# Performance work log

Measured on AMD Instinct MI355X. Metric: run time of the kernel, lower is better.

## Reference

```python
import jax, jax.numpy as jnp
import numpy as np

NH, DK, DV, KC = 12, 64, 128, 4  # heads, head_qk_dim, head_v_dim, conv_size


def causal_dwconv(x, w):
    # x: [B, L, C], w: [C, K] depthwise causal conv (torch Conv1d groups=C with left pad K-1)
    K = w.shape[1]
    L = x.shape[1]
    xp = jnp.pad(x, ((0, 0), (K - 1, 0), (0, 0)))
    out = xp[:, 0:L, :] * w[:, 0]
    for j in range(1, K):
        out = out + xp[:, j:j + L, :] * w[:, j]
    return out


def l2norm(x, eps=1e-12):
    n = jnp.sqrt(jnp.sum(x * x, axis=-1, keepdims=True))
    return x / jnp.maximum(n, eps)


def rmsnorm(x, eps=1e-5):
    return x * jax.lax.rsqrt(jnp.mean(x * x, axis=-1, keepdims=True) + eps)


def setup_inputs() -> dict:
    key = jax.random.key(0)
    ks = jax.random.split(key, 16)
    B, L, H = 4, 2048, 1024
    Kd, Vd = 768, 1536  # key_dim, value_dim
    s = 0.02
    inp = {
        'hidden_states': jax.random.normal(ks[0], (B, L, H), jnp.float32),
        'Wq': jax.random.normal(ks[1], (H, Kd), jnp.float32) * s,
        'Wk': jax.random.normal(ks[2], (H, Kd), jnp.float32) * s,
        'Wv': jax.random.normal(ks[3], (H, Vd), jnp.float32) * s,
        'Wg': jax.random.normal(ks[4], (H, Vd), jnp.float32) * s,
        'Wgk': jax.random.normal(ks[5], (H, NH), jnp.float32) * s,
        'Wb': jax.random.normal(ks[6], (H, NH), jnp.float32) * s,
        'bb': jnp.zeros((NH,), jnp.float32),
        'conv_q': jax.random.normal(ks[7], (Kd, KC), jnp.float32) * 0.3,
        'conv_k': jax.random.normal(ks[8], (Kd, KC), jnp.float32) * 0.3,
        'conv_v': jax.random.normal(ks[9], (Vd, KC), jnp.float32) * 0.3,
        'A_log': jnp.log(jax.random.uniform(ks[10], (NH,), jnp.float32, 1e-4, 16.0)),
        'gnorm_w': jnp.ones((DV,), jnp.float32),
        'Wo': jax.random.normal(ks[11], (Vd, H), jnp.float32) * s,
    }
    dt = jnp.exp(jax.random.uniform(ks[12], (NH,), jnp.float32) * (np.log(0.1) - np.log(0.001)) + np.log(0.001))
    dt = jnp.clip(dt, 1e-4, None)
    inp['dt_bias'] = dt + jnp.log(-jnp.expm1(-dt))
    return inp


def reference(hidden_states, Wq, Wk, Wv, Wg, Wgk, Wb, bb, conv_q, conv_k, conv_v, A_log, dt_bias, gnorm_w, Wo):
    B, L, H = hidden_states.shape
    # projections + causal depthwise short conv with silu (qk_norm='l2')
    q = jax.nn.silu(causal_dwconv(hidden_states @ Wq, conv_q))
    k = jax.nn.silu(causal_dwconv(hidden_states @ Wk, conv_k))
    v = jax.nn.silu(causal_dwconv(hidden_states @ Wv, conv_v))
    # mamba-style decay gate: gk = -exp(A_log) * softplus(x Wgk + dt_bias)  -> [B,L,NH]
    gk = -jnp.exp(A_log) * jax.nn.softplus(hidden_states @ Wgk + dt_bias)
    beta = jax.nn.sigmoid(hidden_states @ Wb + bb)  # [B,L,NH]
    q = l2norm(q.reshape(B, L, NH, DK))
    k = l2norm(k.reshape(B, L, NH, DK))
    v = v.reshape(B, L, NH, DV)

    # gated delta rule recurrence: S_t = exp(gk_t) * S_{t-1}; S_t += k_t (beta_t (v_t - k_t^T S_t)); o_t = q_t^T S_t
    def step(S, inp_t):
        qt, kt, vt, gt, bt = inp_t
        S = S * jnp.exp(gt)[..., None, None]
        pred = jnp.einsum('bhk,bhkv->bhv', kt, S)
        delta = bt[..., None] * (vt - pred)
        S = S + kt[..., None] * delta[:, :, None, :]
        ot = jnp.einsum('bhk,bhkv->bhv', qt, S)
        return S, ot

    xs = (jnp.moveaxis(q, 1, 0), jnp.moveaxis(k, 1, 0), jnp.moveaxis(v, 1, 0),
          jnp.moveaxis(gk, 1, 0), jnp.moveaxis(beta, 1, 0))
    S0 = jnp.zeros((B, NH, DK, DV), hidden_states.dtype)
    _, o = jax.lax.scan(step, S0, xs)
    o = jnp.moveaxis(o, 0, 1)  # [B,L,NH,DV]

    # fused RMSNorm + swish gate, then output projection
    g = (hidden_states @ Wg).reshape(B, L, NH, DV)
    o = rmsnorm(o) * gnorm_w * jax.nn.silu(g)
    return o.reshape(B, L, NH * DV) @ Wo
```

## Files before the change

kernel.cpp:

```cpp
#include <hip/hip_runtime.h>

#define B_   4
#define L_   2048
#define H_   1024
#define KD   768
#define VD   1536
#define NHh  12
#define DKh  64
#define DVh  128
#define M_   (B_ * L_)
#define NC   32
#define NCID (B_ * NHh * NC)

using bf16x8 = __attribute__((ext_vector_type(8))) __bf16;
using f32x4  = __attribute__((ext_vector_type(4))) float;
using ui4    = __attribute__((ext_vector_type(4))) unsigned int;
using f4v    = __attribute__((ext_vector_type(4))) float;
using u16x4  = __attribute__((ext_vector_type(4))) unsigned short;
using u16x8  = __attribute__((ext_vector_type(8))) unsigned short;

__device__ __forceinline__ float bf2f(unsigned short u) {
  unsigned int x = ((unsigned int)u) << 16;
  return __builtin_bit_cast(float, x);
}
__device__ __forceinline__ unsigned short f2bf(float f) {
  unsigned int u = __builtin_bit_cast(unsigned int, f);
  u += 0x7fffu + ((u >> 16) & 1u);
  return (unsigned short)(u >> 16);
}
__device__ __forceinline__ float sigmoidf_(float x) { return 1.f / (1.f + __expf(-x)); }

__device__ __forceinline__ void async_copy16(const unsigned short* __restrict__ g,
                                             unsigned short* l) {
  __builtin_amdgcn_global_load_lds((const __attribute__((address_space(1))) unsigned int*)g,
                                   (__attribute__((address_space(3))) unsigned int*)l, 16, 0, 0);
}

__global__ void detect_dtype(const unsigned short* __restrict__ hs, int* __restrict__ flag) {
  int tid = threadIdx.x;
  int cnt = 0;
  for (int i = tid; i < 1024; i += 256) {
    int e = (hs[i] >> 7) & 0xFF;
    if (e >= 134) cnt++;
  }
  #pragma unroll
  for (int off = 32; off; off >>= 1) cnt += __shfl_xor(cnt, off);
  __shared__ int red[4];
  if ((tid & 63) == 0) red[tid >> 6] = cnt;
  __syncthreads();
  if (tid == 0) *flag = (red[0] + red[1] + red[2] + red[3] > 100) ? 1 : 0;
}

__global__ void convert_hs4(const void* __restrict__ src, unsigned short* __restrict__ dst,
                            const int* __restrict__ flag) {
  size_t i = ((size_t)blockIdx.x * 256 + threadIdx.x) * 4;
  if (*flag) {
    f4v v = *(const f4v*)((const float*)src + i);
    u16x4 o;
    o.x = f2bf(v[0]); o.y = f2bf(v[1]); o.z = f2bf(v[2]); o.w = f2bf(v[3]);
    *(u16x4*)(dst + i) = o;
  } else {
    *(u16x4*)(dst + i) = *(const u16x4*)((const unsigned short*)src + i);
  }
}

__global__ void convert_small(const void* s0, const void* s1, const void* s2,
                              const void* s3, const void* s4, const void* s5, const void* s6,
                              float* d0, float* d1, float* d2, float* d3, float* d4,
                              float* d5, float* d6, const int* __restrict__ flag) {
  const int sizes[7] = {KD * 4, KD * 4, VD * 4, NHh, NHh, NHh, DVh};
  int a = blockIdx.y;
  const void* s; float* d;
  switch (a) {
    case 0: s = s0; d = d0; break;  case 1: s = s1; d = d1; break;
    case 2: s = s2; d = d2; break;  case 3: s = s3; d = d3; break;
    case 4: s = s4; d = d4; break;  case 5: s = s5; d = d5; break;
    default: s = s6; d = d6; break;
  }
  int i = blockIdx.x * 256 + threadIdx.x;
  if (i >= sizes[a]) return;
  float v = (*flag) ? ((const float*)s)[i] : bf2f(((const unsigned short*)s)[i]);
  if (a < 3) {
    int C = (a == 2) ? VD : KD;
    d[(i & 3) * C + (i >> 2)] = v;
  } else {
    d[i] = v;
  }
}

__global__ void transpose_conv(const void* __restrict__ in, unsigned short* __restrict__ out,
                               int R, int C, const int* __restrict__ flag) {
  __shared__ unsigned short tile[32][33];
  int f = *flag;
  int c0 = blockIdx.x * 32, r0 = blockIdx.y * 32;
  int tx = threadIdx.x & 31, ty = threadIdx.x >> 5;
  #pragma unroll
  for (int i = 0; i < 32; i += 8) {
    int r = r0 + ty + i, c = c0 + tx;
    unsigned short v = 0;
    if (r < R && c < C)
      v = f ? f2bf(((const float*)in)[(size_t)r * C + c])
            : ((const unsigned short*)in)[(size_t)r * C + c];
    tile[ty + i][tx] = v;
  }
  __syncthreads();
  #pragma unroll
  for (int i = 0; i < 32; i += 8) {
    int c = c0 + ty + i, r = r0 + tx;
    if (c < C && r < R) out[(size_t)c * R + r] = tile[tx][ty + i];
  }
}

#define BMt 128
#define BNt 128
#define BKt 64

__global__ __launch_bounds__(256, 2) void gemm_bt(
    const unsigned short* __restrict__ Ag,
    const unsigned short* __restrict__ BTg,
    void* __restrict__ Cg,
    int M, int N, int K, int f32mode, const int* __restrict__ flag) {
  __shared__ __align__(16) unsigned short As[2][BMt * BKt];
  __shared__ __align__(16) unsigned short Bs[2][BNt * BKt];
  const int tid = threadIdx.x;
  const int wave = tid >> 6, lane = tid & 63;
  const int wr = wave >> 1, wc = wave & 1;
  const int lrow = lane & 15, lq = lane >> 4;
  const int row0 = blockIdx.x * BMt;
  const int bcol0 = blockIdx.y * BNt;
  unsigned short* Cb = (unsigned short*)Cg;
  int col0 = bcol0, Nst = N;
  if (f32mode == 3) {
    int region = bcol0 / 1536;
    Cb += (size_t)region * (size_t)M_ * 1536;
    col0 = bcol0 - region * 1536;
    Nst = 1536;
  }
  f32x4 acc[4][4] = {};
  auto stage = [&](int sb, int k0) {
    #pragma unroll
    for (int i = 0; i < 4; i++) {
      int c = i * 256 + tid;
      int r = c >> 3;
      int kk = ((c & 7) ^ (r & 7)) << 3;
      int ldsbase = (i * 256 + wave * 64) * 8;
      async_copy16(&Ag[(size_t)(row0 + r) * K + k0 + kk], &As[sb][ldsbase]);
      async_copy16(&BTg[(size_t)(bcol0 + r) * K + k0 + kk], &Bs[sb][ldsbase]);
    }
  };
  stage(0, 0);
  __syncthreads();
  int cur = 0;
  for (int k0 = 0; k0 < K; k0 += BKt) {
    if (k0 + BKt < K) stage(cur ^ 1, k0 + BKt);
    #pragma unroll
    for (int ks = 0; ks < BKt; ks += 32) {
      bf16x8 af[4], bfr[4];
      #pragma unroll
      for (int i = 0; i < 4; i++) {
        int ra = wr * 64 + i * 16 + lrow;
        int sa = ((ks >> 3) + lq) ^ (ra & 7);
        af[i]  = *(const bf16x8*)&As[cur][ra * BKt + (sa << 3)];
        int rb = wc * 64 + i * 16 + lrow;
        int sb2 = ((ks >> 3) + lq) ^ (rb & 7);
        bfr[i] = *(const bf16x8*)&Bs[cur][rb * BKt + (sb2 << 3)];
      }
      #pragma unroll
      for (int mi = 0; mi < 4; mi++)
        #pragma unroll
        for (int ni = 0; ni < 4; ni++)
          acc[mi][ni] = __builtin_amdgcn_mfma_f32_16x16x32_bf16(af[mi], bfr[ni], acc[mi][ni], 0, 0, 0);
    }
    __syncthreads();
    cur ^= 1;
  }
  bool f32 = (f32mode == 1) || (f32mode == 2 && *flag != 0);
  #pragma unroll
  for (int mi = 0; mi < 4; mi++)
    #pragma unroll
    for (int ni = 0; ni < 4; ni++)
      #pragma unroll
      for (int r = 0; r < 4; r++) {
        int rr = row0 + wr * 64 + mi * 16 + lq * 4 + r;
        int cc = col0 + wc * 64 + ni * 16 + lrow;
        float v = acc[mi][ni][r];
        if (f32) ((float*)Cg)[(size_t)rr * N + cc] = v;
        else     Cb[(size_t)rr * Nst + cc] = f2bf(v);
      }
}

__global__ void gkbeta_kernel(const float* __restrict__ logits,
                              const float* __restrict__ bb,
                              const float* __restrict__ A_log,
                              const float* __restrict__ dt_bias,
                              float* __restrict__ gkb, float* __restrict__ betab) {
  int idx = blockIdx.x * 256 + threadIdx.x;
  int m = idx / 24, j = idx - m * 24;
  float x = logits[(size_t)m * 128 + j];
  if (j < 12) {
    float t = x + dt_bias[j];
    float sp = (t > 20.f) ? t : log1pf(__expf(t));
    gkb[m * NHh + j] = -__expf(A_log[j]) * sp;
  } else {
    betab[m * NHh + (j - 12)] = sigmoidf_(x + bb[j - 12]);
  }
}

__global__ __launch_bounds__(192) void conv_qk_kernel(
    const unsigned short* __restrict__ raw, int rstride,
    const float* __restrict__ w,
    unsigned short* __restrict__ outp) {
  int tid = threadIdx.x;
  int rib = tid / 96, within = tid - rib * 96;
  int bl = blockIdx.x * 2 + rib;
  int c = within * 8;
  int l = bl & (L_ - 1);
  float acc[8] = {};
  #pragma unroll
  for (int j = 0; j < 4; j++) {
    int ll = l - 3 + j;
    if (ll >= 0) {
      u16x8 v = *(const u16x8*)&raw[(size_t)(bl - 3 + j) * rstride + c];
      f4v w0 = *(const f4v*)&w[j * KD + c];
      f4v w1 = *(const f4v*)&w[j * KD + c + 4];
      #pragma unroll
      for (int e = 0; e < 4; e++) acc[e] += bf2f(v[e]) * w0[e];
      #pragma unroll
      for (int e = 0; e < 4; e++) acc[4 + e] += bf2f(v[4 + e]) * w1[e];
    }
  }
  float x[8], ss = 0.f;
  #pragma unroll
  for (int e = 0; e < 8; e++) {
    float a = acc[e];
    x[e] = a * sigmoidf_(a);
    ss += x[e] * x[e];
  }
  #pragma unroll
  for (int off = 1; off <= 4; off <<= 1) ss += __shfl_xor(ss, off);
  float inv = 1.f / fmaxf(sqrtf(ss), 1e-12f);
  u16x8 o;
  #pragma unroll
  for (int e = 0; e < 8; e++) o[e] = f2bf(x[e] * inv);
  *(u16x8*)&outp[(size_t)bl * KD + c] = o;
}

__global__ void conv_v_kernel(const unsigned short* __restrict__ raw,
                              const float* __restrict__ w,
                              unsigned short* __restrict__ outp) {
  int idx = blockIdx.x * 256 + threadIdx.x;
  int bl = idx / 192;
  int c = (idx - bl * 192) * 8;
  int l = bl & (L_ - 1);
  float acc[8] = {};
  #pragma unroll
  for (int j = 0; j < 4; j++) {
    int ll = l - 3 + j;
    if (ll >= 0) {
      u16x8 v = *(const u16x8*)&raw[(size_t)(bl - 3 + j) * VD + c];
      f4v w0 = *(const f4v*)&w[j * VD + c];
      f4v w1 = *(const f4v*)&w[j * VD + c + 4];
      #pragma unroll
      for (int e = 0; e < 4; e++) acc[e] += bf2f(v[e]) * w0[e];
      #pragma unroll
      for (int e = 0; e < 4; e++) acc[4 + e] += bf2f(v[4 + e]) * w1[e];
    }
  }
  u16x8 o;
  #pragma unroll
  for (int e = 0; e < 8; e++) {
    float a = acc[e];
    o[e] = f2bf(a * sigmoidf_(a));
  }
  *(u16x8*)&outp[(size_t)bl * VD + c] = o;
}

__global__ __launch_bounds__(256) void phase1_kernel(
    const unsigned short* __restrict__ kb, const unsigned short* __restrict__ vb,
    const float* __restrict__ gkb, const float* __restrict__ betab,
    unsigned short* __restrict__ U0g, unsigned short* __restrict__ Wmg,
    float* __restrict__ Gamg) {
  int cid = blockIdx.x;
  int c = cid & (NC - 1), bh = cid >> 5;
  int h = bh % NHh, b = bh / NHh;
  int bl0 = b * L_ + (c << 6);
  __shared__ __align__(16) unsigned short K_lds[64][72];
  __shared__ __align__(16) unsigned short Ab[64][72];
  __shared__ __align__(16) unsigned short Tb[64][72];
  __shared__ __align__(16) unsigned short TbT[64][72];
  __shared__ __align__(16) unsigned short Qt[64][40];
  __shared__ __align__(16) unsigned short Mpad[16][40];
  __shared__ __align__(16) unsigned short RHSt[192][72];
  __shared__ float G_lds[64], beta_lds[64], besc_lds[64];
  int tid = threadIdx.x;
  int wave = tid >> 6, lane = tid & 63, lq = lane >> 4, lrow = lane & 15;
  {
    u16x4 z = {};
    unsigned short* tb = &Tb[0][0];  unsigned short* tt = &TbT[0][0];
    for (int i = tid * 4; i < 64 * 72; i += 1024) {
      *(u16x4*)&tb[i] = z;  *(u16x4*)&tt[i] = z;
    }
    unsigned short* qt = &Qt[0][0];
    for (int i = tid * 4; i < 64 * 40; i += 1024) *(u16x4*)&qt[i] = z;
    if (tid < 160) *(u16x4*)&(&Mpad[0][0])[tid * 4] = z;
  }
  {
    int j = tid >> 2, d0 = (tid & 3) << 4;
    const ui4* src = (const ui4*)&kb[(size_t)(bl0 + j) * KD + h * 64 + d0];
    *(ui4*)&K_lds[j][d0]     = src[0];
    *(ui4*)&K_lds[j][d0 + 8] = src[1];
  }
  if (tid < 64) {
    float g  = gkb[(size_t)(bl0 + tid) * NHh + h];
    float bt = betab[(size_t)(bl0 + tid) * NHh + h];
    #pragma unroll
    for (int off = 1; off < 64; off <<= 1) {
      int src = lane - off;
      float y = __shfl(g, src < 0 ? 0 : src);
      if (lane >= off) g += y;
    }
    G_lds[tid]    = g;
    beta_lds[tid] = bt;
    besc_lds[tid] = bt * __expf(g);
    Gamg[(size_t)cid * 64 + tid] = g;
  }
  __syncthreads();
  #pragma unroll
  for (int mt = 0; mt < 4; mt++) {
    f32x4 acc = {};
    #pragma unroll
    for (int ks = 0; ks < 2; ks++) {
      bf16x8 a  = *(const bf16x8*)&K_lds[wave * 16 + lrow][ks * 32 + lq * 8];
      bf16x8 b2 = *(const bf16x8*)&K_lds[mt * 16 + lrow][ks * 32 + lq * 8];
      acc = __builtin_amdgcn_mfma_f32_16x16x32_bf16(a, b2, acc, 0, 0, 0);
    }
    #pragma unroll
    for (int r = 0; r < 4; r++) {
      int j = wave * 16 + lq * 4 + r, m = mt * 16 + lrow;
      Ab[j][m] = (m < j) ? f2bf(beta_lds[j] * __expf(G_lds[j] - G_lds[m]) * acc[r])
                         : (unsigned short)0;
    }
  }
  __syncthreads();
  if (wave == 0) {
    int blk = lq, cc = lrow, base = blk * 16;
    float t[16];
    t[0] = (cc == 0) ? 1.f : 0.f;
    #pragma unroll
    for (int j = 1; j < 16; j++) {
      float s = 0.f;
      #pragma unroll
      for (int m = 0; m < j; m++)
        s += bf2f(Ab[base + j][base + m]) * t[m];
      t[j] = ((cc == j) ? 1.f : 0.f) - s;
    }
    #pragma unroll
    for (int j = 0; j < 16; j++) {
      unsigned short bv = f2bf(t[j]);
      Tb[base + j][base + cc]  = bv;
      TbT[base + cc][base + j] = bv;
    }
  } else {
    int r = tid - 64;
    if (r < 128) {
      const unsigned short* vp = &vb[(size_t)bl0 * VD + h * 128 + r];
      for (int j = 0; j < 64; j++)
        RHSt[r][j] = f2bf(beta_lds[j] * bf2f(vp[(size_t)j * VD]));
    } else {
      int d = r - 128;
      for (int j = 0; j < 64; j++)
        RHSt[r][j] = f2bf(besc_lds[j] * bf2f(K_lds[j][d]));
    }
  }
  __syncthreads();
  #pragma unroll
  for (int lvl = 1; lvl < 4; lvl++) {
    {
      int m = tid >> 4, k = tid & 15;
      Ab[lvl * 16 + m][lvl * 16 + k] = 0;
      Mpad[m][k] = Tb[lvl * 16 + m][lvl * 16 + k];
    }
    __syncthreads();
    f32x4 accP = {};
    #pragma unroll
    for (int ks2 = 0; ks2 < 2; ks2++) {
      bf16x8 a  = *(const bf16x8*)&Ab[lvl * 16 + lrow][ks2 * 32 + lq * 8];
      bf16x8 b2 = *(const bf16x8*)&TbT[wave * 16 + lrow][ks2 * 32 + lq * 8];
      accP = __builtin_amdgcn_mfma_f32_16x16x32_bf16(a, b2, accP, 0, 0, 0);
    }
    {
      int col = wave * 16 + lrow;
      u16x4 qp;
      #pragma unroll
      for (int r = 0; r < 4; r++) {
        int krow = lq * 4 + r;
        float e = (col == lvl * 16 + krow) ? 1.f : 0.f;
        ((unsigned short*)&qp)[r] = f2bf(e - accP[r]);
      }
      *(u16x4*)&Qt[col][lq * 4] = qp;
    }
    __syncthreads();
    {
      bf16x8 am = *(const bf16x8*)&Mpad[lrow][lq * 8];
      bf16x8 bq = *(const bf16x8*)&Qt[wave * 16 + lrow][lq * 8];
      f32x4 accR = {};
      accR = __builtin_amdgcn_mfma_f32_16x16x32_bf16(am, bq, accR, 0, 0, 0);
      #pragma unroll
      for (int r = 0; r < 4; r++) {
        int row = lvl * 16 + lq * 4 + r, col = wave * 16 + lrow;
        unsigned short bv = f2bf(accR[r]);
        Tb[row][col]  = bv;
        TbT[col][row] = bv;
      }
    }
    __syncthreads();
  }
  bf16x8 af0 = *(const bf16x8*)&Tb[wave * 16 + lrow][lq * 8];
  bf16x8 af1 = *(const bf16x8*)&Tb[wave * 16 + lrow][32 + lq * 8];
  #pragma unroll
  for (int nt = 0; nt < 12; nt++) {
    f32x4 acc = {};
    bf16x8 b0 = *(const bf16x8*)&RHSt[nt * 16 + lrow][lq * 8];
    bf16x8 b1 = *(const bf16x8*)&RHSt[nt * 16 + lrow][32 + lq * 8];
    acc = __builtin_amdgcn_mfma_f32_16x16x32_bf16(af0, b0, acc, 0, 0, 0);
    acc = __builtin_amdgcn_mfma_f32_16x16x32_bf16(af1, b1, acc, 0, 0, 0);
    #pragma unroll
    for (int r = 0; r < 4; r++) {
      int i = wave * 16 + lq * 4 + r;
      int col = nt * 16 + lrow;
      if (nt < 8) U0g[(size_t)cid * 8192 + i * 128 + col] = f2bf(acc[r]);
      else        Wmg[(size_t)cid * 4096 + i * 64 + (col - 128)] = f2bf(acc[r]);
    }
  }
}

__global__ __launch_bounds__(256) void phase2_kernel(
    const unsigned short* __restrict__ kb,
    const unsigned short* __restrict__ U0g, const unsigned short* __restrict__ Wmg,
    const float* __restrict__ Gamg, unsigned short* __restrict__ P0g) {
  int blk = blockIdx.x;
  int vc = blk & 3, bh = blk >> 2;
  int h = bh % NHh, b = bh / NHh;
  __shared__ __align__(16) unsigned short P_bf[32][72];
  __shared__ __align__(16) unsigned short Wm_lds[64][72];
  __shared__ __align__(16) unsigned short Ktmp[64][72];
  __shared__ __align__(16) unsigned short KpT_lds[64][72];
  __shared__ __align__(16) unsigned short U0_lds[64][40];
  __shared__ __align__(16) unsigned short UT_lds[32][72];
  __shared__ float G2[64];
  int tid = threadIdx.x;
  int wave = tid >> 6, lane = tid & 63, lq = lane >> 4, lrow = lane & 15;
  int vt = wave & 1, dbase = (wave >> 1) * 2;
  f32x4 P[2] = {};
  int pj = tid >> 2, px = (tid & 3) << 4;
  int pv = (tid & 3) << 3;
  ui4 pf_wm0, pf_wm1, pf_k0, pf_k1, pf_u0;
  float pf_g = 0.f;
  {
    size_t cid0 = (size_t)bh * NC;
    int bl0 = b * L_;
    pf_wm0 = *(const ui4*)&Wmg[cid0 * 4096 + pj * 64 + px];
    pf_wm1 = *(const ui4*)&Wmg[cid0 * 4096 + pj * 64 + px + 8];
    pf_k0  = *(const ui4*)&kb[(size_t)(bl0 + pj) * KD + h * 64 + px];
    pf_k1  = *(const ui4*)&kb[(size_t)(bl0 + pj) * KD + h * 64 + px + 8];
    pf_u0  = *(const ui4*)&U0g[cid0 * 8192 + pj * 128 + vc * 32 + pv];
    if (tid < 64) pf_g = Gamg[cid0 * 64 + tid];
  }
  for (int c = 0; c < NC; c++) {
    size_t cid = (size_t)bh * NC + c;
    #pragma unroll
    for (int di = 0; di < 2; di++)
      #pragma unroll
      for (int r = 0; r < 4; r++)
        P_bf[vt * 16 + lq * 4 + r][(dbase + di) * 16 + lrow] = f2bf(P[di][r]);
    *(ui4*)&Wm_lds[pj][px]     = pf_wm0;
    *(ui4*)&Wm_lds[pj][px + 8] = pf_wm1;
    *(ui4*)&Ktmp[pj][px]       = pf_k0;
    *(ui4*)&Ktmp[pj][px + 8]   = pf_k1;
    *(ui4*)&U0_lds[pj][pv]     = pf_u0;
    if (tid < 64) G2[tid] = pf_g;
    __syncthreads();
    float gend = __expf(G2[63]);
    {
      int v = tid >> 3, d8 = (tid & 7) << 3;
      *(ui4*)&P0g[cid * 8192 + (size_t)(vc * 32 + v) * 64 + d8] = *(const ui4*)&P_bf[v][d8];
    }
    if (c + 1 < NC) {
      size_t cid1 = cid + 1;
      int bl1 = b * L_ + ((c + 1) << 6);
      pf_wm0 = *(const ui4*)&Wmg[cid1 * 4096 + pj * 64 + px];
      pf_wm1 = *(const ui4*)&Wmg[cid1 * 4096 + pj * 64 + px + 8];
      pf_k0  = *(const ui4*)&kb[(size_t)(bl1 + pj) * KD + h * 64 + px];
      pf_k1  = *(const ui4*)&kb[(size_t)(bl1 + pj) * KD + h * 64 + px + 8];
      pf_u0  = *(const ui4*)&U0g[cid1 * 8192 + pj * 128 + vc * 32 + pv];
      if (tid < 64) pf_g = Gamg[cid1 * 64 + tid];
    }
    {
      int d = tid & 63, j0 = (tid >> 6) << 4;
      float Ge = G2[63];
      #pragma unroll
      for (int i = 0; i < 16; i++) {
        int j = j0 + i;
        KpT_lds[d][j] = f2bf(__expf(Ge - G2[j]) * bf2f(Ktmp[j][d]));
      }
    }
    #pragma unroll
    for (int vt2 = 0; vt2 < 2; vt2++) {
      f32x4 acc = {};
      #pragma unroll
      for (int ks2 = 0; ks2 < 2; ks2++) {
        bf16x8 a  = *(const bf16x8*)&Wm_lds[wave * 16 + lrow][ks2 * 32 + lq * 8];
        bf16x8 b2 = *(const bf16x8*)&P_bf[vt2 * 16 + lrow][ks2 * 32 + lq * 8];
        acc = __builtin_amdgcn_mfma_f32_16x16x32_bf16(a, b2, acc, 0, 0, 0);
      }
      u16x4 p;
      #pragma unroll
      for (int r = 0; r < 4; r++) {
        int j = wave * 16 + lq * 4 + r;
        ((unsigned short*)&p)[r] = f2bf(bf2f(U0_lds[j][vt2 * 16 + lrow]) - acc[r]);
      }
      *(u16x4*)&UT_lds[vt2 * 16 + lrow][wave * 16 + lq * 4] = p;
    }
    __syncthreads();
    #pragma unroll
    for (int di = 0; di < 2; di++) {
      f32x4 acc = P[di];
      #pragma unroll
      for (int r = 0; r < 4; r++) acc[r] *= gend;
      #pragma unroll
      for (int ks2 = 0; ks2 < 2; ks2++) {
        bf16x8 a  = *(const bf16x8*)&UT_lds[vt * 16 + lrow][ks2 * 32 + lq * 8];
        bf16x8 b2 = *(const bf16x8*)&KpT_lds[(dbase + di) * 16 + lrow][ks2 * 32 + lq * 8];
        acc = __builtin_amdgcn_mfma_f32_16x16x32_bf16(a, b2, acc, 0, 0, 0);
      }
      P[di] = acc;
    }
  }
}

__global__ __launch_bounds__(256) void phase3_kernel(
    const unsigned short* __restrict__ qb, const unsigned short* __restrict__ kb,
    const unsigned short* __restrict__ U0g, const unsigned short* __restrict__ Wmg,
    const unsigned short* __restrict__ P0g, const float* __restrict__ Gamg,
    unsigned short* __restrict__ o_raw) {
  int cid = blockIdx.x;
  int c = cid & (NC - 1), bh = cid >> 5;
  int h = bh % NHh, b = bh / NHh;
  int bl0 = b * L_ + (c << 6);
  __shared__ __align__(16) unsigned short Q_lds[64][72];
  __shared__ __align__(16) unsigned short K_lds[64][72];
  __shared__ __align__(16) unsigned short WM_lds[64][72];
  __shared__ __align__(16) unsigned short P0_lds[128][72];
  __shared__ __align__(16) unsigned short U0_lds[64][128];
  __shared__ __align__(16) unsigned short UT_lds[128][72];
  __shared__ float G_lds[64];
  int tid = threadIdx.x;
  int wave = tid >> 6, lane = tid & 63, lq = lane >> 4, lrow = lane & 15;
  {
    int j = tid >> 2, d0 = (tid & 3) << 4;
    const ui4* qs = (const ui4*)&qb[(size_t)(bl0 + j) * KD + h * 64 + d0];
    *(ui4*)&Q_lds[j][d0] = qs[0];  *(ui4*)&Q_lds[j][d0 + 8] = qs[1];
    const ui4* ks = (const ui4*)&kb[(size_t)(bl0 + j) * KD + h * 64 + d0];
    *(ui4*)&K_lds[j][d0] = ks[0];  *(ui4*)&K_lds[j][d0 + 8] = ks[1];
    const ui4* ws = (const ui4*)&Wmg[(size_t)cid * 4096 + j * 64 + d0];
    *(ui4*)&WM_lds[j][d0] = ws[0]; *(ui4*)&WM_lds[j][d0 + 8] = ws[1];
    int v = tid >> 1, e0 = (tid & 1) << 5;
    const ui4* ps = (const ui4*)&P0g[(size_t)cid * 8192 + v * 64 + e0];
    *(ui4*)&P0_lds[v][e0]      = ps[0]; *(ui4*)&P0_lds[v][e0 + 8]  = ps[1];
    *(ui4*)&P0_lds[v][e0 + 16] = ps[2]; *(ui4*)&P0_lds[v][e0 + 24] = ps[3];
    int e1 = tid * 32;
    const ui4* us = (const ui4*)&U0g[(size_t)cid * 8192 + e1];
    ui4* ud = (ui4*)&U0_lds[0][e1];
    ud[0] = us[0]; ud[1] = us[1]; ud[2] = us[2]; ud[3] = us[3];
    if (tid < 64) G_lds[tid] = Gamg[(size_t)cid * 64 + tid];
  }
  __syncthreads();
  #pragma unroll
  for (int nt = 0; nt < 8; nt++) {
    f32x4 acc = {};
    #pragma unroll
    for (int ks2 = 0; ks2 < 2; ks2++) {
      bf16x8 a  = *(const bf16x8*)&WM_lds[wave * 16 + lrow][ks2 * 32 + lq * 8];
      bf16x8 b2 = *(const bf16x8*)&P0_lds[nt * 16 + lrow][ks2 * 32 + lq * 8];
      acc = __builtin_amdgcn_mfma_f32_16x16x32_bf16(a, b2, acc, 0, 0, 0);
    }
    u16x4 p;
    #pragma unroll
    for (int r = 0; r < 4; r++) {
      int j = wave * 16 + lq * 4 + r;
      ((unsigned short*)&p)[r] = f2bf(bf2f(U0_lds[j][nt * 16 + lrow]) - acc[r]);
    }
    *(u16x4*)&UT_lds[nt * 16 + lrow][wave * 16 + lq * 4] = p;
  }
  __syncthreads();
  #pragma unroll
  for (int mt = 0; mt < 4; mt++) {
    f32x4 acc = {};
    #pragma unroll
    for (int ks2 = 0; ks2 < 2; ks2++) {
      bf16x8 a  = *(const bf16x8*)&Q_lds[wave * 16 + lrow][ks2 * 32 + lq * 8];
      bf16x8 b2 = *(const bf16x8*)&K_lds[mt * 16 + lrow][ks2 * 32 + lq * 8];
      acc = __builtin_amdgcn_mfma_f32_16x16x32_bf16(a, b2, acc, 0, 0, 0);
    }
    #pragma unroll
    for (int r = 0; r < 4; r++) {
      int i = wave * 16 + lq * 4 + r, j = mt * 16 + lrow;
      WM_lds[i][j] = (j <= i) ? f2bf(__expf(G_lds[i] - G_lds[j]) * acc[r]) : (unsigned short)0;
    }
  }
  __syncthreads();
  #pragma unroll
  for (int nt = 0; nt < 8; nt++) {
    f32x4 accO = {}, accS = {};
    #pragma unroll
    for (int ks2 = 0; ks2 < 2; ks2++) {
      bf16x8 aM = *(const bf16x8*)&WM_lds[wave * 16 + lrow][ks2 * 32 + lq * 8];
      bf16x8 bU = *(const bf16x8*)&UT_lds[nt * 16 + lrow][ks2 * 32 + lq * 8];
      accO = __builtin_amdgcn_mfma_f32_16x16x32_bf16(aM, bU, accO, 0, 0, 0);
      bf16x8 aQ = *(const bf16x8*)&Q_lds[wave * 16 + lrow][ks2 * 32 + lq * 8];
      bf16x8 bP = *(const bf16x8*)&P0_lds[nt * 16 + lrow][ks2 * 32 + lq * 8];
      accS = __builtin_amdgcn_mfma_f32_16x16x32_bf16(aQ, bP, accS, 0, 0, 0);
    }
    #pragma unroll
    for (int r = 0; r < 4; r++) {
      int i = wave * 16 + lq * 4 + r;
      float o = accO[r] + __expf(G_lds[i]) * accS[r];
      o_raw[(size_t)(bl0 + i) * VD + h * 128 + nt * 16 + lrow] = f2bf(o);
    }
  }
}

__global__ void norm_gate_kernel(unsigned short* __restrict__ o_raw,
                                 const unsigned short* __restrict__ g,
                                 const float* __restrict__ gnw) {
  int tid = threadIdx.x;
  int r = blockIdx.x * 16 + (tid >> 4);
  int v = (tid & 15) * 8;
  u16x8 xo = *(const u16x8*)&o_raw[(size_t)r * DVh + v];
  u16x8 xg = *(const u16x8*)&g[(size_t)r * DVh + v];
  float x[8], ss = 0.f;
  #pragma unroll
  for (int e = 0; e < 8; e++) {
    x[e] = bf2f(xo[e]);
    ss += x[e] * x[e];
  }
  #pragma unroll
  for (int off = 1; off <= 8; off <<= 1) ss += __shfl_xor(ss, off);
  float inv = rsqrtf(ss * (1.f / (float)DVh) + 1e-5f);
  f4v w0 = *(const f4v*)&gnw[v];
  f4v w1 = *(const f4v*)&gnw[v + 4];
  u16x8 o;
  #pragma unroll
  for (int e = 0; e < 8; e++) {
    float gv = bf2f(xg[e]);
    float wv = (e < 4) ? w0[e] : w1[e - 4];
    o[e] = f2bf(x[e] * inv * wv * (gv * sigmoidf_(gv)));
  }
  *(u16x8*)&o_raw[(size_t)r * DVh + v] = o;
}

extern "C" void kernel_launch(void* const* d_in, const int* in_sizes, int n_in,
                              void* d_out, int out_size, void* d_ws, size_t ws_size,
                              hipStream_t stream) {
  const void* hs      = d_in[0];
  const void* Wq      = d_in[1];
  const void* Wk      = d_in[2];
  const void* Wv      = d_in[3];
  const void* Wg      = d_in[4];
  const void* Wgk     = d_in[5];
  const void* Wb      = d_in[6];
  const void* bb      = d_in[7];
  const void* cq      = d_in[8];
  const void* ck      = d_in[9];
  const void* cv      = d_in[10];
  const void* A_log   = d_in[11];
  const void* gnorm_w = d_in[12];
  const void* Wo      = d_in[13];
  const void* dt_bias = d_in[14];

  char* wsB = (char*)d_ws;
  size_t off = 0;
  auto walloc = [&](size_t bytes) -> char* {
    char* p = wsB + off;
    off += (bytes + 1023) & ~(size_t)1023;
    return p;
  };
  int* flag = (int*)walloc(1024);
  unsigned short* WqT   = (unsigned short*)walloc((size_t)KD * H_ * 2);
  unsigned short* WkT   = (unsigned short*)walloc((size_t)KD * H_ * 2);
  unsigned short* WvT   = (unsigned short*)walloc((size_t)VD * H_ * 2);
  unsigned short* WgT   = (unsigned short*)walloc((size_t)VD * H_ * 2);
  unsigned short* WgkbT = (unsigned short*)walloc((size_t)128 * H_ * 2);
  unsigned short* WoT   = (unsigned short*)walloc((size_t)H_ * VD * 2);
  float* cqf   = (float*)walloc((size_t)KD * 4 * 4);
  float* ckf   = (float*)walloc((size_t)KD * 4 * 4);
  float* cvf   = (float*)walloc((size_t)VD * 4 * 4);
  float* bbf   = (float*)walloc(NHh * 4);
  float* A_logf= (float*)walloc(NHh * 4);
  float* dtf   = (float*)walloc(NHh * 4);
  float* gnwf  = (float*)walloc(DVh * 4);
  float* gkb   = (float*)walloc((size_t)M_ * NHh * 4);
  float* betab = (float*)walloc((size_t)M_ * NHh * 4);
  float* Gamg  = (float*)walloc((size_t)NCID * 64 * 4);
  unsigned short* c_hs  = (unsigned short*)walloc((size_t)M_ * H_ * 2);
  unsigned short* qkraw = (unsigned short*)walloc((size_t)M_ * 1536 * 2);
  unsigned short* vraw  = (unsigned short*)walloc((size_t)M_ * VD * 2);
  unsigned short* gbuf  = (unsigned short*)walloc((size_t)M_ * VD * 2);
  unsigned short* qb    = (unsigned short*)walloc((size_t)M_ * KD * 2);
  unsigned short* kb    = (unsigned short*)walloc((size_t)M_ * KD * 2);
  unsigned short* vb    = (unsigned short*)walloc((size_t)M_ * VD * 2);
  float*          logits32 = (float*)vraw;
  unsigned short* Wmg   = c_hs;
  unsigned short* U0g   = qkraw;
  unsigned short* o_raw = vraw;
  unsigned short* P0g   = vb;

  detect_dtype<<<1, 256, 0, stream>>>((const unsigned short*)hs, flag);
  convert_small<<<dim3(24, 7), 256, 0, stream>>>(cq, ck, cv, bb, A_log, dt_bias, gnorm_w,
                                                 cqf, ckf, cvf, bbf, A_logf, dtf, gnwf, flag);
  transpose_conv<<<dim3(KD / 32, H_ / 32), 256, 0, stream>>>(Wq, WqT, H_, KD, flag);
  transpose_conv<<<dim3(KD / 32, H_ / 32), 256, 0, stream>>>(Wk, WkT, H_, KD, flag);
  transpose_conv<<<dim3(VD / 32, H_ / 32), 256, 0, stream>>>(Wv, WvT, H_, VD, flag);
  transpose_conv<<<dim3(VD / 32, H_ / 32), 256, 0, stream>>>(Wg, WgT, H_, VD, flag);
  transpose_conv<<<dim3(1, H_ / 32), 256, 0, stream>>>(Wgk, WgkbT, H_, NHh, flag);
  transpose_conv<<<dim3(1, H_ / 32), 256, 0, stream>>>(Wb, WgkbT + 12 * H_, H_, NHh, flag);
  transpose_conv<<<dim3(H_ / 32, VD / 32), 256, 0, stream>>>(Wo, WoT, VD, H_, flag);
  convert_hs4<<<(M_ * H_) / 1024, 256, 0, stream>>>(hs, c_hs, flag);

  gemm_bt<<<dim3(M_ / 128, 1), 256, 0, stream>>>(c_hs, WgkbT, logits32, M_, 128, H_, 1, flag);
  gkbeta_kernel<<<(M_ * 24) / 256, 256, 0, stream>>>(logits32, bbf, A_logf, dtf, gkb, betab);
  gemm_bt<<<dim3(M_ / 128, 4608 / 128), 256, 0, stream>>>(c_hs, WqT, qkraw, M_, 4608, H_, 3, flag);

  conv_qk_kernel<<<M_ / 2, 192, 0, stream>>>(qkraw, 1536, cqf, qb);
  conv_qk_kernel<<<M_ / 2, 192, 0, stream>>>(qkraw + KD, 1536, ckf, kb);
  conv_v_kernel<<<(M_ * 192) / 256, 256, 0, stream>>>(vraw, cvf, vb);

  phase1_kernel<<<NCID, 256, 0, stream>>>(kb, vb, gkb, betab, U0g, Wmg, Gamg);
  phase2_kernel<<<B_ * NHh * 4, 256, 0, stream>>>(kb, U0g, Wmg, Gamg, P0g);
  phase3_kernel<<<NCID, 256, 0, stream>>>(qb, kb, U0g, Wmg, P0g, Gamg, o_raw);

  norm_gate_kernel<<<(M_ * NHh) / 16, 256, 0, stream>>>(o_raw, gbuf, gnwf);

  gemm_bt<<<dim3(M_ / 128, H_ / 128), 256, 0, stream>>>(o_raw, WoT, d_out, M_, H_, VD, 2, flag);
}
```

Measured before the change: 456.2 us.

## Add 256-row GEMM kernel with deeper prefetch for QKVG and output projections

Adds a templated 512-thread GEMM with 256xBN tiles (BN 256 for the fused QKVG projection, 128 for the output projection). Loads are issued two tiles ahead, with explicit vmcnt waits and raw barriers in place of __syncthreads, and setprio is raised around the MFMA block. Larger tiles raise operand reuse per LDS load and cut redundant global traffic, at the cost of more accumulator registers (up to 128 floats per lane) and possible occupancy loss. The small gk/beta GEMM stays on the old kernel, which is simplified to drop the region-split store path.

```diff
diff --git a/kernel.cpp b/kernel.cpp
--- a/kernel.cpp
+++ b/kernel.cpp
@@ -128,6 +128,76 @@
   const int lrow = lane & 15, lq = lane >> 4;
   const int row0 = blockIdx.x * BMt;
   const int bcol0 = blockIdx.y * BNt;
+  f32x4 acc[4][4] = {};
+  auto stage = [&](int sb, int k0) {
+    #pragma unroll
+    for (int i = 0; i < 4; i++) {
+      int c = i * 256 + tid;
+      int r = c >> 3;
+      int kk = ((c & 7) ^ (r & 7)) << 3;
+      int ldsbase = (i * 256 + wave * 64) * 8;
+      async_copy16(&Ag[(size_t)(row0 + r) * K + k0 + kk], &As[sb][ldsbase]);
+      async_copy16(&BTg[(size_t)(bcol0 + r) * K + k0 + kk], &Bs[sb][ldsbase]);
+    }
+  };
+  stage(0, 0);
+  __syncthreads();
+  int cur = 0;
+  for (int k0 = 0; k0 < K; k0 += BKt) {
+    if (k0 + BKt < K) stage(cur ^ 1, k0 + BKt);
+    #pragma unroll
+    for (int ks = 0; ks < BKt; ks += 32) {
+      bf16x8 af[4], bfr[4];
+      #pragma unroll
+      for (int i = 0; i < 4; i++) {
+        int ra = wr * 64 + i * 16 + lrow;
+        int sa = ((ks >> 3) + lq) ^ (ra & 7);
+        af[i]  = *(const bf16x8*)&As[cur][ra * BKt + (sa << 3)];
+        int rb = wc * 64 + i * 16 + lrow;
+        int sb2 = ((ks >> 3) + lq) ^ (rb & 7);
+        bfr[i] = *(const bf16x8*)&Bs[cur][rb * BKt + (sb2 << 3)];
+      }
+      #pragma unroll
+      for (int mi = 0; mi < 4; mi++)
+        #pragma unroll
+        for (int ni = 0; ni < 4; ni++)
+          acc[mi][ni] = __builtin_amdgcn_mfma_f32_16x16x32_bf16(af[mi], bfr[ni], acc[mi][ni], 0, 0, 0);
+    }
+    __syncthreads();
+    cur ^= 1;
+  }
+  bool f32 = (f32mode == 1) || (f32mode == 2 && *flag != 0);
+  #pragma unroll
+  for (int mi = 0; mi < 4; mi++)
+    #pragma unroll
+    for (int ni = 0; ni < 4; ni++)
+      #pragma unroll
+      for (int r = 0; r < 4; r++) {
+        int rr = row0 + wr * 64 + mi * 16 + lq * 4 + r;
+        int cc = bcol0 + wc * 64 + ni * 16 + lrow;
+        float v = acc[mi][ni][r];
+        if (f32) ((float*)Cg)[(size_t)rr * N + cc] = v;
+        else     ((unsigned short*)Cg)[(size_t)rr * N + cc] = f2bf(v);
+      }
+}
+
+template<int BNq>
+__global__ __launch_bounds__(512, 2) void gemm256(
+    const unsigned short* __restrict__ Ag,
+    const unsigned short* __restrict__ BTg,
+    void* __restrict__ Cg,
+    int M, int N, int K, int f32mode, const int* __restrict__ flag) {
+  constexpr int BM = 256, BK = 64;
+  constexpr int NF = BNq / 64;
+  constexpr int NLD = 4 + NF;
+  __shared__ __align__(16) unsigned short As[2][BM * BK];
+  __shared__ __align__(16) unsigned short Bs[2][BNq * BK];
+  const int tid = threadIdx.x;
+  const int wave = tid >> 6, lane = tid & 63;
+  const int wr = wave >> 2, wc = wave & 3;
+  const int lrow = lane & 15, lq = lane >> 4;
+  const int row0 = blockIdx.x * BM;
+  const int bcol0 = blockIdx.y * BNq;
   unsigned short* Cb = (unsigned short*)Cg;
   int col0 = bcol0, Nst = N;
   if (f32mode == 3) {
@@ -136,53 +206,69 @@
     col0 = bcol0 - region * 1536;
     Nst = 1536;
   }
-  f32x4 acc[4][4] = {};
+  f32x4 acc[8][NF] = {};
   auto stage = [&](int sb, int k0) {
     #pragma unroll
     for (int i = 0; i < 4; i++) {
-      int c = i * 256 + tid;
+      int c = i * 512 + tid;
       int r = c >> 3;
       int kk = ((c & 7) ^ (r & 7)) << 3;
-      int ldsbase = (i * 256 + wave * 64) * 8;
-      async_copy16(&Ag[(size_t)(row0 + r) * K + k0 + kk], &As[sb][ldsbase]);
-      async_copy16(&BTg[(size_t)(bcol0 + r) * K + k0 + kk], &Bs[sb][ldsbase]);
+      async_copy16(&Ag[(size_t)(row0 + r) * K + k0 + kk],
+                   &As[sb][(i * 512 + wave * 64) * 8]);
+    }
+    #pragma unroll
+    for (int i = 0; i < NF; i++) {
+      int c = i * 512 + tid;
+      int r = c >> 3;
+      int kk = ((c & 7) ^ (r & 7)) << 3;
+      async_copy16(&BTg[(size_t)(bcol0 + r) * K + k0 + kk],
+                   &Bs[sb][(i * 512 + wave * 64) * 8]);
     }
   };
+  const int NT = K / BK;
   stage(0, 0);
-  __syncthreads();
+  stage(1, BK);
   int cur = 0;
-  for (int k0 = 0; k0 < K; k0 += BKt) {
-    if (k0 + BKt < K) stage(cur ^ 1, k0 + BKt);
-    #pragma unroll
-    for (int ks = 0; ks < BKt; ks += 32) {
-      bf16x8 af[4], bfr[4];
-      #pragma unroll
-      for (int i = 0; i < 4; i++) {
-        int ra = wr * 64 + i * 16 + lrow;
-        int sa = ((ks >> 3) + lq) ^ (ra & 7);
-        af[i]  = *(const bf16x8*)&As[cur][ra * BKt + (sa << 3)];
-        int rb = wc * 64 + i * 16 + lrow;
-        int sb2 = ((ks >> 3) + lq) ^ (rb & 7);
-        bfr[i] = *(const bf16x8*)&Bs[cur][rb * BKt + (sb2 << 3)];
-      }
-      #pragma unroll
-      for (int mi = 0; mi < 4; mi++)
+  for (int t = 0; t < NT; t++) {
+    if (t + 1 < NT) asm volatile("s_waitcnt vmcnt(%0)" :: "i"(NLD) : "memory");
+    else            asm volatile("s_waitcnt vmcnt(0)" ::: "memory");
+    __builtin_amdgcn_s_barrier();
+    #pragma unroll
+    for (int ks = 0; ks < 2; ks++) {
+      bf16x8 af[8], bfv[NF];
+      #pragma unroll
+      for (int i = 0; i < 8; i++) {
+        int ra = wr * 128 + i * 16 + lrow;
+        int sa = ((ks << 2) + lq) ^ (ra & 7);
+        af[i] = *(const bf16x8*)&As[cur][ra * BK + (sa << 3)];
+      }
+      #pragma unroll
+      for (int i = 0; i < NF; i++) {
+        int rb = wc * (BNq / 4) + i * 16 + lrow;
+        int sb2 = ((ks << 2) + lq) ^ (rb & 7);
+        bfv[i] = *(const bf16x8*)&Bs[cur][rb * BK + (sb2 << 3)];
+      }
+      __builtin_amdgcn_s_setprio(1);
+      #pragma unroll
+      for (int mi = 0; mi < 8; mi++)
         #pragma unroll
-        for (int ni = 0; ni < 4; ni++)
-          acc[mi][ni] = __builtin_amdgcn_mfma_f32_16x16x32_bf16(af[mi], bfr[ni], acc[mi][ni], 0, 0, 0);
-    }
-    __syncthreads();
+        for (int ni = 0; ni < NF; ni++)
+          acc[mi][ni] = __builtin_amdgcn_mfma_f32_16x16x32_bf16(af[mi], bfv[ni], acc[mi][ni], 0, 0, 0);
+      __builtin_amdgcn_s_setprio(0);
+    }
+    __builtin_amdgcn_s_barrier();
+    if (t + 2 < NT) stage(cur, (t + 2) * BK);
     cur ^= 1;
   }
   bool f32 = (f32mode == 1) || (f32mode == 2 && *flag != 0);
   #pragma unroll
-  for (int mi = 0; mi < 4; mi++)
-    #pragma unroll
-    for (int ni = 0; ni < 4; ni++)
+  for (int mi = 0; mi < 8; mi++)
+    #pragma unroll
+    for (int ni = 0; ni < NF; ni++)
       #pragma unroll
       for (int r = 0; r < 4; r++) {
-        int rr = row0 + wr * 64 + mi * 16 + lq * 4 + r;
-        int cc = col0 + wc * 64 + ni * 16 + lrow;
+        int rr = row0 + wr * 128 + mi * 16 + lq * 4 + r;
+        int cc = col0 + wc * (BNq / 4) + ni * 16 + lrow;
         float v = acc[mi][ni][r];
         if (f32) ((float*)Cg)[(size_t)rr * N + cc] = v;
         else     Cb[(size_t)rr * Nst + cc] = f2bf(v);
@@ -729,7 +815,7 @@
 
   gemm_bt<<<dim3(M_ / 128, 1), 256, 0, stream>>>(c_hs, WgkbT, logits32, M_, 128, H_, 1, flag);
   gkbeta_kernel<<<(M_ * 24) / 256, 256, 0, stream>>>(logits32, bbf, A_logf, dtf, gkb, betab);
-  gemm_bt<<<dim3(M_ / 128, 4608 / 128), 256, 0, stream>>>(c_hs, WqT, qkraw, M_, 4608, H_, 3, flag);
+  gemm256<256><<<dim3(M_ / 256, 4608 / 256), 512, 0, stream>>>(c_hs, WqT, qkraw, M_, 4608, H_, 3, flag);
 
   conv_qk_kernel<<<M_ / 2, 192, 0, stream>>>(qkraw, 1536, cqf, qb);
   conv_qk_kernel<<<M_ / 2, 192, 0, stream>>>(qkraw + KD, 1536, ckf, kb);
@@ -741,5 +827,5 @@
 
   norm_gate_kernel<<<(M_ * NHh) / 16, 256, 0, stream>>>(o_raw, gbuf, gnwf);
 
-  gemm_bt<<<dim3(M_ / 128, H_ / 128), 256, 0, stream>>>(o_raw, WoT, d_out, M_, H_, VD, 2, flag);
-}
+  gemm256<128><<<dim3(M_ / 256, H_ / 128), 512, 0, stream>>>(o_raw, WoT, d_out, M_, H_, VD, 2, flag);
+}
```

After: 478.2 us. 1.05x slower.
